# Kernel optimization log

Hardware: AMD Instinct MI355X
Metric: run time of the kernel (lower is better)

Reference implementation:

```python
import math
import jax
import jax.numpy as jnp
import numpy as np

N_IMG = 8
A = 3
H = 100
W = 100
STRIDE = 16
IMG = 1600
PRE_NMS_TOP_N = 2000
POST_NMS_TOP_N = 1000
NMS_THRESH = 0.7
MIN_SIZE = 0
BBOX_XFORM_CLIP = math.log(1000.0 / 16.0)


def setup_inputs() -> dict:
    key = jax.random.key(0)
    k1, k2 = jax.random.split(key)
    objectness = jax.random.normal(k1, (N_IMG, A, H, W), jnp.float32)
    box_regression = jax.random.normal(k2, (N_IMG, A * 4, H, W), jnp.float32) * 0.5
    # Grid anchors, flattened in (H, W, A) order to match objectness.permute(0,2,3,1)
    cy = (jnp.arange(H, dtype=jnp.float32) + 0.5) * STRIDE  # [H]
    cx = (jnp.arange(W, dtype=jnp.float32) + 0.5) * STRIDE  # [W]
    half = jnp.array([64.0, 128.0, 256.0], jnp.float32) / 2.0  # [A]
    cy = cy[:, None, None]  # [H,1,1]
    cx = cx[None, :, None]  # [1,W,1]
    s = half[None, None, :]  # [1,1,A]
    x1, y1, x2, y2 = jnp.broadcast_arrays(cx - s, cy - s, cx + s, cy + s)
    anc = jnp.stack([x1, y1, x2, y2], axis=-1).reshape(-1, 4)  # [H*W*A, 4]
    anchors = jnp.broadcast_to(anc[None], (N_IMG, H * W * A, 4)).copy()
    return {
        "objectness": objectness,
        "box_regression": box_regression,
        "anchors": anchors,
        "image_height": IMG,
        "image_width": IMG,
    }


def _decode(deltas, boxes):
    # BoxCoder(weights=(1,1,1,1)).decode with TO_REMOVE=1
    widths = boxes[..., 2] - boxes[..., 0] + 1.0
    heights = boxes[..., 3] - boxes[..., 1] + 1.0
    ctr_x = boxes[..., 0] + 0.5 * widths
    ctr_y = boxes[..., 1] + 0.5 * heights
    dx, dy = deltas[..., 0], deltas[..., 1]
    dw = jnp.minimum(deltas[..., 2], BBOX_XFORM_CLIP)
    dh = jnp.minimum(deltas[..., 3], BBOX_XFORM_CLIP)
    pcx = dx * widths + ctr_x
    pcy = dy * heights + ctr_y
    pw = jnp.exp(dw) * widths
    ph = jnp.exp(dh) * heights
    return jnp.stack(
        [pcx - 0.5 * pw, pcy - 0.5 * ph, pcx + 0.5 * pw - 1.0, pcy + 0.5 * ph - 1.0],
        axis=-1,
    )


def _nms_keep(boxes, valid, thresh):
    # boxes [n,4] sorted by descending score; valid: pre-filter mask.
    n = boxes.shape[0]
    x1, y1, x2, y2 = boxes[:, 0], boxes[:, 1], boxes[:, 2], boxes[:, 3]
    areas = (x2 - x1 + 1.0) * (y2 - y1 + 1.0)
    xx1 = jnp.maximum(x1[:, None], x1[None, :])
    yy1 = jnp.maximum(y1[:, None], y1[None, :])
    xx2 = jnp.minimum(x2[:, None], x2[None, :])
    yy2 = jnp.minimum(y2[:, None], y2[None, :])
    inter = jnp.maximum(xx2 - xx1 + 1.0, 0.0) * jnp.maximum(yy2 - yy1 + 1.0, 0.0)
    iou = inter / (areas[:, None] + areas[None, :] - inter)
    idx = jnp.arange(n)

    def body(i, keep):
        sup = keep[i] & (iou[i] > thresh) & (idx > i)
        return keep & ~sup

    return jax.lax.fori_loop(0, n, body, valid)


def _forward(objectness, box_regression, anchors, image_height, image_width):
    N, A_, H_, W_ = objectness.shape
    scores = jax.nn.sigmoid(objectness.transpose(0, 2, 3, 1).reshape(N, -1))  # [N, A*H*W]
    deltas = (
        box_regression.reshape(N, A_, 4, H_, W_)
        .transpose(0, 3, 4, 1, 2)
        .reshape(N, -1, 4)
    )
    pre = min(PRE_NMS_TOP_N, scores.shape[1])
    top_scores, top_idx = jax.lax.top_k(scores, pre)  # sorted descending
    deltas = jnp.take_along_axis(deltas, top_idx[:, :, None], axis=1)
    anc = jnp.take_along_axis(anchors, top_idx[:, :, None], axis=1)
    props = _decode(deltas, anc)  # [N, pre, 4]
    # clip to image (fact = 1)
    xs = jnp.clip(props[..., 0::2], 0.0, image_width - 1.0)
    ys = jnp.clip(props[..., 1::2], 0.0, image_height - 1.0)
    props = jnp.stack([xs[..., 0], ys[..., 0], xs[..., 1], ys[..., 1]], axis=-1)
    # filter small / out-of-image-center boxes
    ws = props[..., 2] - props[..., 0] + 1.0
    hs = props[..., 3] - props[..., 1] + 1.0
    xc = props[..., 0] + ws / 2.0
    yc = props[..., 1] + hs / 2.0
    valid = (ws >= MIN_SIZE) & (hs >= MIN_SIZE) & (xc < image_width) & (yc < image_height)
    keep = jax.vmap(lambda b, v: _nms_keep(b, v, NMS_THRESH))(props, valid)

    def _select(b, s, k):
        # compact kept boxes (already score-sorted) into fixed-size output
        rank = jnp.cumsum(k) - 1
        tgt = jnp.where(k & (rank < POST_NMS_TOP_N), rank, POST_NMS_TOP_N)
        ob = jnp.zeros((POST_NMS_TOP_N + 1, 4), b.dtype).at[tgt].set(b)[:POST_NMS_TOP_N]
        os = jnp.zeros((POST_NMS_TOP_N + 1,), s.dtype).at[tgt].set(s)[:POST_NMS_TOP_N]
        ov = jnp.arange(POST_NMS_TOP_N) < jnp.minimum(jnp.sum(k), POST_NMS_TOP_N)
        return ob, os, ov

    return jax.vmap(_select)(props, top_scores, keep)


def reference(objectness, box_regression, anchors, image_height, image_width):
    # Returns (boxes [N,post,4], objectness scores [N,post], valid mask [N,post])
    return _forward(objectness, box_regression, anchors, image_height, image_width)
```

## Files before the change

### kernel.cpp

```cpp
#include <hip/hip_runtime.h>
#include <math.h>
#include <stdint.h>

#define NIMG   8
#define NA     30000
#define NQ4    7500
#define PRE_N  2000
#define POST_N 1000
#define NMS_TH 0.7f
#define DCLIP  4.135166556742356f
#define IMGF   1600.0f
#define IMGM1  1599.0f
#define CAND_MAX 4096
#define HPITCH 4104
#define BIG_BIN 64
#define PREF_BIN 3064u


__device__ __forceinline__ void decode_store(
    uint64_t key, unsigned int rank, int n, const float* __restrict__ breg,
    float* __restrict__ wsBoxes, float* __restrict__ wsScores,
    int* __restrict__ wsValid)
{
    unsigned int idx = (unsigned int)key;
    unsigned int k   = ~((unsigned int)(key >> 32));
    unsigned int u   = (k & 0x80000000u) ? (k & 0x7fffffffu) : ~k;
    float logit = __uint_as_float(u);
    float score = 1.0f / (1.0f + expf(-logit));

    int a = idx % 3, t = idx / 3, w = t % 100, h = t / 100;
    const float* bp = breg + n*120000 + (a*4)*10000 + t;
    float dx = bp[0], dy = bp[10000], dw = bp[20000], dh = bp[30000];

    float half = (a == 0) ? 32.0f : ((a == 1) ? 64.0f : 128.0f);
    float cx = w * 16.0f + 8.0f, cy = h * 16.0f + 8.0f;
    float x1 = cx - half, y1 = cy - half, x2 = cx + half, y2 = cy + half;
    float wd = x2 - x1 + 1.0f, hg = y2 - y1 + 1.0f;
    float cxr = x1 + 0.5f * wd, cyr = y1 + 0.5f * hg;
    dw = fminf(dw, DCLIP); dh = fminf(dh, DCLIP);
    float pcx = dx * wd + cxr, pcy = dy * hg + cyr;
    float pw = expf(dw) * wd, ph = expf(dh) * hg;
    float px1 = pcx - 0.5f * pw, py1 = pcy - 0.5f * ph;
    float px2 = pcx + 0.5f * pw - 1.0f, py2 = pcy + 0.5f * ph - 1.0f;
    px1 = fminf(fmaxf(px1, 0.0f), IMGM1);
    px2 = fminf(fmaxf(px2, 0.0f), IMGM1);
    py1 = fminf(fmaxf(py1, 0.0f), IMGM1);
    py2 = fminf(fmaxf(py2, 0.0f), IMGM1);
    float wss = px2 - px1 + 1.0f, hss = py2 - py1 + 1.0f;
    float xc = px1 + wss * 0.5f, yc = py1 + hss * 0.5f;
    int valid = (wss >= 0.0f) && (hss >= 0.0f) && (xc < IMGF) && (yc < IMGF);

    ((float4*)wsBoxes)[n * PRE_N + (int)rank] = make_float4(px1, py1, px2, py2);
    wsScores[n * PRE_N + (int)rank] = score;
    wsValid [n * PRE_N + (int)rank] = valid;
}

__device__ __forceinline__ unsigned int keyof(float f) {
    unsigned int u = __float_as_uint(f);
    return (u & 0x80000000u) ? ~u : (u | 0x80000000u);
}

__global__ __launch_bounds__(1024) void topk_decode(
    const float* __restrict__ obj, const float* __restrict__ breg,
    float* __restrict__ wsBoxes, float* __restrict__ wsScores,
    int* __restrict__ wsValid)
{
    const int n    = blockIdx.x;
    const int tid  = threadIdx.x;
    const int lane = tid & 63;
    const int wid  = tid >> 6;
    const int rep  = wid & 3;

    __shared__ unsigned int   histf[4 * HPITCH];
    __shared__ unsigned short sufx[4096];
    __shared__ uint64_t       grp[CAND_MAX];
    __shared__ uint64_t       grp2[CAND_MAX];
    __shared__ unsigned int   wsum[16];
    __shared__ unsigned int   sbstar;
    __shared__ unsigned int   lbbase[16];
    __shared__ unsigned int   lbcnt, lbtot;

    unsigned int*   hist2  = histf;
    unsigned short* sufx2  = (unsigned short*)(histf + HPITCH);
    unsigned char*  bin2lb = (unsigned char*)(histf + 2 * HPITCH);

    for (int b = tid; b < 4 * HPITCH; b += 1024) histf[b] = 0u;
    __syncthreads();

    const float4* obj4 = (const float4*)(obj + n * NA);
    float4 v[8];
    #pragma unroll
    for (int kk = 0; kk < 7; ++kk) v[kk] = obj4[tid + kk * 1024];
    v[7] = make_float4(0.f, 0.f, 0.f, 0.f);
    if (tid < NQ4 - 7 * 1024) v[7] = obj4[tid + 7 * 1024];

    #pragma unroll
    for (int kk = 0; kk < 8; ++kk) {
        if (kk == 7 && tid >= NQ4 - 7 * 1024) continue;
        const float fv[4] = {v[kk].x, v[kk].y, v[kk].z, v[kk].w};
        #pragma unroll
        for (int e = 0; e < 4; ++e) {
            unsigned int b = keyof(fv[e]) >> 20;
            if (b >= PREF_BIN)
                atomicAdd(&histf[rep * HPITCH + b], 1u);
        }
    }
    __syncthreads();

    unsigned int c0, c1, c2, c3;
    {
        const int b0 = tid * 4;
        c0 = histf[b0+0] + histf[HPITCH+b0+0] + histf[2*HPITCH+b0+0] + histf[3*HPITCH+b0+0];
        c1 = histf[b0+1] + histf[HPITCH+b0+1] + histf[2*HPITCH+b0+1] + histf[3*HPITCH+b0+1];
        c2 = histf[b0+2] + histf[HPITCH+b0+2] + histf[2*HPITCH+b0+2] + histf[3*HPITCH+b0+2];
        c3 = histf[b0+3] + histf[HPITCH+b0+3] + histf[2*HPITCH+b0+3] + histf[3*HPITCH+b0+3];
    }
    unsigned int p = c0 + c1 + c2 + c3;
    unsigned int s = p;
    #pragma unroll
    for (int off = 1; off < 64; off <<= 1) {
        unsigned int vv = __shfl_down(s, off);
        if (lane + off < 64) s += vv;
    }
    if (lane == 0) wsum[wid] = s;
    __syncthreads();
    unsigned int ftotal = 0;
    for (int w = 0; w < 16; ++w) ftotal += wsum[w];

    if (ftotal < PRE_N) {
        #pragma unroll
        for (int kk = 0; kk < 8; ++kk) {
            if (kk == 7 && tid >= NQ4 - 7 * 1024) continue;
            const float fv[4] = {v[kk].x, v[kk].y, v[kk].z, v[kk].w};
            #pragma unroll
            for (int e = 0; e < 4; ++e) {
                unsigned int b = keyof(fv[e]) >> 20;
                if (b < PREF_BIN)
                    atomicAdd(&histf[rep * HPITCH + b], 1u);
            }
        }
        __syncthreads();
        {
            const int b0 = tid * 4;
            c0 = histf[b0+0] + histf[HPITCH+b0+0] + histf[2*HPITCH+b0+0] + histf[3*HPITCH+b0+0];
            c1 = histf[b0+1] + histf[HPITCH+b0+1] + histf[2*HPITCH+b0+1] + histf[3*HPITCH+b0+1];
            c2 = histf[b0+2] + histf[HPITCH+b0+2] + histf[2*HPITCH+b0+2] + histf[3*HPITCH+b0+2];
            c3 = histf[b0+3] + histf[HPITCH+b0+3] + histf[2*HPITCH+b0+3] + histf[3*HPITCH+b0+3];
        }
        p = c0 + c1 + c2 + c3;
        s = p;
        #pragma unroll
        for (int off = 1; off < 64; off <<= 1) {
            unsigned int vv = __shfl_down(s, off);
            if (lane + off < 64) s += vv;
        }
        __syncthreads();
        if (lane == 0) wsum[wid] = s;
        __syncthreads();
    }

    unsigned int wafter = 0;
    for (int w = wid + 1; w < 16; ++w) wafter += wsum[w];
    unsigned int after = (s - p) + wafter;
    {
        unsigned int S3 = after + c3;
        unsigned int S2 = S3 + c2;
        unsigned int S1 = S2 + c1;
        unsigned int S0 = S1 + c0;
        if (S3 >= PRE_N && after < PRE_N) { sbstar = tid*4+3; }
        if (S2 >= PRE_N && S3    < PRE_N) { sbstar = tid*4+2; }
        if (S1 >= PRE_N && S2    < PRE_N) { sbstar = tid*4+1; }
        if (S0 >= PRE_N && S1    < PRE_N) { sbstar = tid*4+0; }
        sufx[tid*4+0] = (unsigned short)S1;
        sufx[tid*4+1] = (unsigned short)S2;
        sufx[tid*4+2] = (unsigned short)S3;
        sufx[tid*4+3] = (unsigned short)after;

        const unsigned int st[4] = {S1, S2, S3, after};
        #pragma unroll
        for (int q = 0; q < 4; ++q) {
            const int b = tid*4 + q;
            unsigned int base = st[q];
            #pragma unroll
            for (int r = 0; r < 4; ++r) {
                unsigned int c = histf[r * HPITCH + b];
                histf[r * HPITCH + b] = base;
                base += c;
            }
        }
    }
    __syncthreads();
    const unsigned int bstar = sbstar;

    #pragma unroll
    for (int kk = 0; kk < 8; ++kk) {
        if (kk == 7 && tid >= NQ4 - 7 * 1024) continue;
        const float fv[4] = {v[kk].x, v[kk].y, v[kk].z, v[kk].w};
        #pragma unroll
        for (int e = 0; e < 4; ++e) {
            unsigned int k = keyof(fv[e]);
            unsigned int b = k >> 20;
            if (b < bstar) continue;
            int j = (tid + kk * 1024) * 4 + e;
            int a = j / 10000, t = j - a * 10000;
            uint64_t key = (((uint64_t)(~k)) << 32) | (unsigned int)(t * 3 + a);
            unsigned int slot = atomicAdd(&histf[rep * HPITCH + b], 1u);
            if (slot < CAND_MAX) grp[slot] = key;
        }
    }
    __syncthreads();

    const unsigned int total = min(histf[3 * HPITCH + bstar], (unsigned int)CAND_MAX);

    ((unsigned int*)bin2lb)[tid] = 0xFFFFFFFFu;
    hist2[tid] = 0u; hist2[tid+1024] = 0u; hist2[tid+2048] = 0u; hist2[tid+3072] = 0u;
    if (tid == 0) { lbcnt = 0u; lbtot = 0u; }
    __syncthreads();

    #pragma unroll
    for (int q = 0; q < 4; ++q) {
        const unsigned int b = (unsigned int)(tid*4 + q);
        if (b >= bstar) {
            const unsigned int ge  = min(histf[3*HPITCH + b], (unsigned int)CAND_MAX);
            const unsigned int cnt = ge - (unsigned int)sufx[b];
            if (cnt > (unsigned int)BIG_BIN) {
                unsigned int pos = atomicAdd(&lbcnt, 1u);
                if (pos < 16u) {
                    bin2lb[b] = (unsigned char)pos;
                    lbbase[pos] = atomicAdd(&lbtot, cnt);
                }
            }
        }
    }
    __syncthreads();

    for (unsigned int slot = tid; slot < total; slot += 1024) {
        const unsigned int hi = (unsigned int)(grp[slot] >> 32);
        const unsigned int b  = 4095u - (hi >> 20);
        const unsigned char lb = bin2lb[b];
        if (lb != 0xFFu)
            atomicAdd(&hist2[(unsigned int)lb * 256u + ((hi >> 12) & 0xFFu)], 1u);
    }
    __syncthreads();

    {
        const unsigned int nlb = min(lbcnt, 16u);
        if ((unsigned int)wid < nlb) {
            const int xb = wid * 256 + lane * 4;
            unsigned int e0 = hist2[xb+0], e1 = hist2[xb+1],
                         e2 = hist2[xb+2], e3 = hist2[xb+3];
            unsigned int tsum = e0 + e1 + e2 + e3;
            unsigned int inc = tsum;
            #pragma unroll
            for (int off = 1; off < 64; off <<= 1) {
                unsigned int vv = __shfl_up(inc, off);
                if (lane >= off) inc += vv;
            }
            unsigned int base = lbbase[wid] + (inc - tsum);
            hist2[xb+0] = base;             sufx2[xb+0] = (unsigned short)base;
            base += e0; hist2[xb+1] = base; sufx2[xb+1] = (unsigned short)base;
            base += e1; hist2[xb+2] = base; sufx2[xb+2] = (unsigned short)base;
            base += e2; hist2[xb+3] = base; sufx2[xb+3] = (unsigned short)base;
        }
    }
    __syncthreads();

    for (unsigned int slot = tid; slot < total; slot += 1024) {
        const uint64_t key = grp[slot];
        const unsigned int hi = (unsigned int)(key >> 32);
        const unsigned int b  = 4095u - (hi >> 20);
        const unsigned char lb = bin2lb[b];
        if (lb != 0xFFu) {
            unsigned int d = atomicAdd(&hist2[(unsigned int)lb * 256u + ((hi >> 12) & 0xFFu)], 1u);
            grp2[d] = key;
        }
    }
    __syncthreads();

    for (unsigned int slot = tid; slot < total; slot += 1024) {
        const uint64_t key = grp[slot];
        const unsigned int hi = (unsigned int)(key >> 32);
        const unsigned int b  = 4095u - (hi >> 20);
        const unsigned int gbeg = sufx[b];
        const unsigned int gend = min(histf[3 * HPITCH + b], (unsigned int)CAND_MAX);
        const unsigned char lb  = bin2lb[b];
        unsigned int rank;

        if (lb != 0xFFu) {
            const unsigned int x   = (unsigned int)lb * 256u + ((hi >> 12) & 0xFFu);
            const unsigned int s2  = sufx2[x];
            const unsigned int e2v = hist2[x];
            rank = gbeg + (s2 - lbbase[lb]);
            for (unsigned int g = s2; g < e2v; g += 8u) {
                #pragma unroll
                for (int i = 0; i < 8; ++i) {
                    const unsigned int gi = g + (unsigned int)i;
                    const uint64_t vv = grp2[min(gi, e2v - 1u)];
                    rank += (gi < e2v && vv < key) ? 1u : 0u;
                }
            }
        } else {
            rank = gbeg;
            unsigned int g = gbeg;
            for (; g + 8u <= gend; g += 8u) {
                uint64_t v0 = grp[g+0], v1 = grp[g+1], v2 = grp[g+2], v3 = grp[g+3];
                uint64_t v4 = grp[g+4], v5 = grp[g+5], v6 = grp[g+6], v7 = grp[g+7];
                unsigned int r0 = (v0 < key) ? 1u : 0u;
                r0 += (v1 < key) ? 1u : 0u;
                r0 += (v2 < key) ? 1u : 0u;
                r0 += (v3 < key) ? 1u : 0u;
                r0 += (v4 < key) ? 1u : 0u;
                r0 += (v5 < key) ? 1u : 0u;
                r0 += (v6 < key) ? 1u : 0u;
                r0 += (v7 < key) ? 1u : 0u;
                rank += r0;
            }
            for (; g < gend; ++g)
                rank += (grp[g] < key) ? 1u : 0u;
        }
        if (rank >= PRE_N) continue;
        decode_store(key, rank, n, breg, wsBoxes, wsScores, wsValid);
    }
}

__global__ __launch_bounds__(512) void nms_mask(
    const float* __restrict__ wsBoxes, uint64_t* __restrict__ mask)
{
    const int blk  = blockIdx.x;
    const int n    = blk >> 5;
    const int i_t  = blk & 31;
    const int tid  = threadIdx.x;
    const int lane = tid & 63;
    const int wv   = tid >> 6;

    __shared__ uint64_t tile[64 * 33];

    for (int idx = tid; idx < 64 * 33; idx += 512) tile[idx] = 0ull;
    __syncthreads();

    const int r = i_t * 64 + lane;
    float4 rb = (r < PRE_N) ? ((const float4*)wsBoxes)[n * PRE_N + r]
                            : make_float4(0.f, 0.f, 0.f, 0.f);
    float ra = (rb.z - rb.x + 1.0f) * (rb.w - rb.y + 1.0f);

    for (int j_t = i_t + wv; j_t < 32; j_t += 8) {
        const int j = j_t * 64 + lane;
        float4 cb = (j < PRE_N) ? ((const float4*)wsBoxes)[n * PRE_N + j]
                                : make_float4(3e30f, 3e30f, 3e30f, 3e30f);
        float ca = (cb.z - cb.x + 1.0f) * (cb.w - cb.y + 1.0f);
        const uint64_t jmask = (j_t == 31) ? 0xFFFFull : ~0ull;
        const bool diag = (j_t == i_t);
        uint64_t myword = 0ull;

        #pragma unroll
        for (int c = 0; c < 64; ++c) {
            float rx1 = __int_as_float(__builtin_amdgcn_readlane(__float_as_int(rb.x), c));
            float ry1 = __int_as_float(__builtin_amdgcn_readlane(__float_as_int(rb.y), c));
            float rx2 = __int_as_float(__builtin_amdgcn_readlane(__float_as_int(rb.z), c));
            float ry2 = __int_as_float(__builtin_amdgcn_readlane(__float_as_int(rb.w), c));
            float rar = __int_as_float(__builtin_amdgcn_readlane(__float_as_int(ra), c));
            float xx1 = fmaxf(rx1, cb.x), yy1 = fmaxf(ry1, cb.y);
            float xx2 = fminf(rx2, cb.z), yy2 = fminf(ry2, cb.w);
            float ww = fmaxf(xx2 - xx1 + 1.0f, 0.0f);
            float hh = fmaxf(yy2 - yy1 + 1.0f, 0.0f);
            float inter = ww * hh;
            float denom = rar + ca - inter;
            unsigned long long bits = __ballot(inter > NMS_TH * denom) & jmask;
            if (diag) bits &= (c == 63) ? 0ull : ((~0ull) << (c + 1));
            if (lane == c) myword = bits;
        }
        tile[lane * 33 + j_t] = myword;
    }
    __syncthreads();

    uint64_t* mrow = mask + ((size_t)n * PRE_N + (size_t)i_t * 64) * 32;
    const int cmax = (i_t == 31) ? 16 : 64;
    for (int idx = tid; idx < cmax * 32; idx += 512) {
        const int rr = idx >> 5, w = idx & 31;
        mrow[idx] = tile[rr * 33 + w];
    }
}

__global__ __launch_bounds__(512) void nms_scan_select(
    const float* __restrict__ wsBoxes, const float* __restrict__ wsScores,
    const int* __restrict__ wsValid, const uint64_t* __restrict__ mask,
    float* __restrict__ out)
{
    const int n    = blockIdx.x;
    const int tid  = threadIdx.x;
    const int lane = tid & 63;
    const int wid  = tid >> 6;

    __shared__ unsigned int sup[64];
    __shared__ unsigned int kml, kmh;
    __shared__ int skept, sdone;
    __shared__ int sscan[256];

    if (tid < 64) sup[tid] = 0u;
    if (tid == 0) { skept = 0; sdone = 0; }
    __syncthreads();

    if (tid < 500) {
        int4 vv = ((const int4*)(wsValid + n * PRE_N))[tid];
        unsigned int nib = (vv.x ? 0u : 1u) | ((vv.y ? 0u : 1u) << 1)
                         | ((vv.z ? 0u : 1u) << 2) | ((vv.w ? 0u : 1u) << 3);
        if (nib) atomicOr(&sup[tid >> 3], nib << ((tid & 7) * 4));
    } else {
        atomicOr(&sup[tid >> 3], 0xFu << ((tid & 7) * 4));
    }
    __syncthreads();

    const uint64_t* mrow = mask + (size_t)n * PRE_N * 32;

    unsigned int cl = 0u, ch = 0u;
    if (wid == 0) {
        uint64_t cw = (lane < PRE_N) ? mrow[(size_t)lane * 32 + 0] : 0ull;
        cl = (unsigned int)cw; ch = (unsigned int)(cw >> 32);
    }

    for (int g = 0; g < 32; ++g) {
        __syncthreads();
        if (sdone) break;

        if (wid == 0) {
            unsigned int nl = 0u, nh = 0u;
            if (g < 31) {
                const int r = (g + 1) * 64 + lane;
                uint64_t cw = (r < PRE_N) ? mrow[(size_t)r * 32 + (g + 1)] : 0ull;
                nl = (unsigned int)cw; nh = (unsigned int)(cw >> 32);
            }

            unsigned long long win =
                ((unsigned long long)sup[2*g + 1] << 32) | sup[2*g];
            #pragma unroll
            for (int b = 0; b < 64; ++b) {
                unsigned long long t =
                    ((unsigned long long)(unsigned int)__builtin_amdgcn_readlane((int)ch, b) << 32)
                    | (unsigned int)__builtin_amdgcn_readlane((int)cl, b);
                unsigned long long dead = (win >> b) & 1ull;
                win |= t & (dead - 1ull);
            }
            unsigned long long km = ~win;
            if (lane == 0) {
                sup[2*g]     = (unsigned int)win;
                sup[2*g + 1] = (unsigned int)(win >> 32);
                kml = (unsigned int)km;
                kmh = (unsigned int)(km >> 32);
                int nk = skept + __popcll(km);
                skept = nk;
                if (nk >= POST_N) sdone = 1;
            }
            cl = nl; ch = nh;
        }
        __syncthreads();

        if (!sdone) {
            const int w = tid & 31;
            if (w > g) {
                const unsigned long long km =
                    ((unsigned long long)kmh << 32) | kml;
                const int r0 = (tid >> 5) * 4;
                unsigned long long acc = 0ull;
                #pragma unroll
                for (int q = 0; q < 4; ++q) {
                    const int rl = r0 + q;
                    if ((km >> rl) & 1ull)
                        acc |= mrow[(size_t)(g * 64 + rl) * 32 + w];
                }
                if (acc) {
                    atomicOr(&sup[2*w],     (unsigned int)acc);
                    atomicOr(&sup[2*w + 1], (unsigned int)(acc >> 32));
                }
            }
        }
    }
    __syncthreads();

    int c[8];
    int lsum = 0;
    const int base8 = tid * 8;
    if (tid < 256) {
        for (int q = 0; q < 8; ++q) {
            const int i = base8 + q;
            c[q] = (i < PRE_N) ? (int)((~sup[i >> 5] >> (i & 31)) & 1u) : 0;
            lsum += c[q];
        }
        sscan[tid] = lsum;
    }
    __syncthreads();
    for (int off = 1; off < 256; off <<= 1) {
        int v = 0;
        if (tid < 256 && tid >= off) v = sscan[tid - off];
        __syncthreads();
        if (tid < 256) sscan[tid] += v;
        __syncthreads();
    }
    const int excl  = (tid < 256) ? (sscan[tid] - lsum) : 0;
    const int total = sscan[255];

    float* ob  = out + n * POST_N * 4;
    float* osc = out + NIMG * POST_N * 4 + n * POST_N;
    float* ovd = out + NIMG * POST_N * 5 + n * POST_N;

    for (int i = tid; i < POST_N * 4; i += 512) ob[i] = 0.0f;
    for (int i = tid; i < POST_N; i += 512) osc[i] = 0.0f;
    const int lim = min(total, POST_N);
    for (int i = tid; i < POST_N; i += 512) ovd[i] = (i < lim) ? 1.0f : 0.0f;
    __syncthreads();

    if (tid < 256) {
        int run = excl;
        for (int q = 0; q < 8; ++q) {
            const int i = base8 + q;
            if (i < PRE_N && c[q]) {
                if (run < POST_N) {
                    float4 b = ((const float4*)wsBoxes)[n * PRE_N + i];
                    ob[run * 4 + 0] = b.x;
                    ob[run * 4 + 1] = b.y;
                    ob[run * 4 + 2] = b.z;
                    ob[run * 4 + 3] = b.w;
                    osc[run] = wsScores[n * PRE_N + i];
                }
                run++;
            }
        }
    }
}

extern "C" void kernel_launch(void* const* d_in, const int* in_sizes, int n_in,
                              void* d_out, int out_size, void* d_ws, size_t ws_size,
                              hipStream_t stream) {
    const float* obj  = (const float*)d_in[0];
    const float* breg = (const float*)d_in[1];
    float* ws        = (float*)d_ws;
    float* wsBoxes   = ws;
    float* wsScores  = ws + 64000;
    int*   wsValid   = (int*)(ws + 80000);
    uint64_t* wsMask = (uint64_t*)(ws + 96000);

    topk_decode<<<NIMG, 1024, 0, stream>>>(obj, breg, wsBoxes, wsScores, wsValid);
    nms_mask<<<NIMG * 32, 512, 0, stream>>>(wsBoxes, wsMask);
    nms_scan_select<<<NIMG, 512, 0, stream>>>(wsBoxes, wsScores, wsValid, wsMask,
                                              (float*)d_out);
}
```

Baseline: 169.5 us.

## Prefetch NMS mask rows one group ahead and hand-code serial scan in scalar asm

Each thread now loads its four mask words for the next 64-row group one iteration early, so the global loads overlap the serial suppression scan instead of stalling after the barrier. The 64-step serial scan over the diagonal block is written as inline scalar assembly (readlane, bitcmp, cselect, and/or) to keep the running window in SGPRs and avoid 64-bit vector emulation. The prefetch loads every mask word unconditionally rather than only the kept rows, and the inline asm adds maintenance and correctness risk.

```diff
diff --git a/kernel.cpp b/kernel.cpp
--- a/kernel.cpp
+++ b/kernel.cpp
@@ -381,6 +381,26 @@
     }
 }
 
+#define NSA(b) \
+    "v_readlane_b32 %[tlo], %[cl], " #b "\n\t" \
+    "v_readlane_b32 %[thi], %[ch], " #b "\n\t" \
+    "s_bitcmp1_b32 %[wlo], " #b "\n\t" \
+    "s_cselect_b32 %[m], 0, -1\n\t" \
+    "s_and_b32 %[tlo], %[tlo], %[m]\n\t" \
+    "s_and_b32 %[thi], %[thi], %[m]\n\t" \
+    "s_or_b32 %[wlo], %[wlo], %[tlo]\n\t" \
+    "s_or_b32 %[whi], %[whi], %[thi]\n\t"
+
+#define NSB(b, c) \
+    "v_readlane_b32 %[tlo], %[cl], " #b "\n\t" \
+    "v_readlane_b32 %[thi], %[ch], " #b "\n\t" \
+    "s_bitcmp1_b32 %[whi], " #c "\n\t" \
+    "s_cselect_b32 %[m], 0, -1\n\t" \
+    "s_and_b32 %[tlo], %[tlo], %[m]\n\t" \
+    "s_and_b32 %[thi], %[thi], %[m]\n\t" \
+    "s_or_b32 %[wlo], %[wlo], %[tlo]\n\t" \
+    "s_or_b32 %[whi], %[whi], %[thi]\n\t"
+
 __global__ __launch_bounds__(512) void nms_scan_select(
     const float* __restrict__ wsBoxes, const float* __restrict__ wsScores,
     const int* __restrict__ wsValid, const uint64_t* __restrict__ mask,
@@ -412,6 +432,15 @@
 
     const uint64_t* mrow = mask + (size_t)n * PRE_N * 32;
 
+    const int r0 = (tid >> 5) * 4;
+    const int w  = tid & 31;
+    uint64_t pfc[4], pfn[4];
+    #pragma unroll
+    for (int q = 0; q < 4; ++q) {
+        const int r = r0 + q;
+        pfn[q] = (w > 0 && r < PRE_N) ? mrow[(size_t)r * 32 + w] : 0ull;
+    }
+
     unsigned int cl = 0u, ch = 0u;
     if (wid == 0) {
         uint64_t cw = (lane < PRE_N) ? mrow[(size_t)lane * 32 + 0] : 0ull;
@@ -421,6 +450,16 @@
     for (int g = 0; g < 32; ++g) {
         __syncthreads();
         if (sdone) break;
+
+        #pragma unroll
+        for (int q = 0; q < 4; ++q) pfc[q] = pfn[q];
+        if (g < 31) {
+            #pragma unroll
+            for (int q = 0; q < 4; ++q) {
+                const int r = (g + 1) * 64 + r0 + q;
+                pfn[q] = (w > g + 1 && r < PRE_N) ? mrow[(size_t)r * 32 + w] : 0ull;
+            }
+        }
 
         if (wid == 0) {
             unsigned int nl = 0u, nh = 0u;
@@ -430,23 +469,33 @@
                 nl = (unsigned int)cw; nh = (unsigned int)(cw >> 32);
             }
 
-            unsigned long long win =
-                ((unsigned long long)sup[2*g + 1] << 32) | sup[2*g];
-            #pragma unroll
-            for (int b = 0; b < 64; ++b) {
-                unsigned long long t =
-                    ((unsigned long long)(unsigned int)__builtin_amdgcn_readlane((int)ch, b) << 32)
-                    | (unsigned int)__builtin_amdgcn_readlane((int)cl, b);
-                unsigned long long dead = (win >> b) & 1ull;
-                win |= t & (dead - 1ull);
-            }
-            unsigned long long km = ~win;
+            unsigned int wlo = (unsigned int)__builtin_amdgcn_readfirstlane((int)sup[2*g]);
+            unsigned int whi = (unsigned int)__builtin_amdgcn_readfirstlane((int)sup[2*g+1]);
+            int tlo_, thi_, m_;
+            asm volatile(
+                NSA(0)  NSA(1)  NSA(2)  NSA(3)  NSA(4)  NSA(5)  NSA(6)  NSA(7)
+                NSA(8)  NSA(9)  NSA(10) NSA(11) NSA(12) NSA(13) NSA(14) NSA(15)
+                NSA(16) NSA(17) NSA(18) NSA(19) NSA(20) NSA(21) NSA(22) NSA(23)
+                NSA(24) NSA(25) NSA(26) NSA(27) NSA(28) NSA(29) NSA(30) NSA(31)
+                NSB(32,0)  NSB(33,1)  NSB(34,2)  NSB(35,3)
+                NSB(36,4)  NSB(37,5)  NSB(38,6)  NSB(39,7)
+                NSB(40,8)  NSB(41,9)  NSB(42,10) NSB(43,11)
+                NSB(44,12) NSB(45,13) NSB(46,14) NSB(47,15)
+                NSB(48,16) NSB(49,17) NSB(50,18) NSB(51,19)
+                NSB(52,20) NSB(53,21) NSB(54,22) NSB(55,23)
+                NSB(56,24) NSB(57,25) NSB(58,26) NSB(59,27)
+                NSB(60,28) NSB(61,29) NSB(62,30) NSB(63,31)
+                : [wlo]"+s"(wlo), [whi]"+s"(whi),
+                  [tlo]"=&s"(tlo_), [thi]"=&s"(thi_), [m]"=&s"(m_)
+                : [cl]"v"(cl), [ch]"v"(ch)
+                : "scc");
+
             if (lane == 0) {
-                sup[2*g]     = (unsigned int)win;
-                sup[2*g + 1] = (unsigned int)(win >> 32);
-                kml = (unsigned int)km;
-                kmh = (unsigned int)(km >> 32);
-                int nk = skept + __popcll(km);
+                sup[2*g]     = wlo;
+                sup[2*g + 1] = whi;
+                unsigned int kl = ~wlo, kh = ~whi;
+                kml = kl; kmh = kh;
+                int nk = skept + __popc(kl) + __popc(kh);
                 skept = nk;
                 if (nk >= POST_N) sdone = 1;
             }
@@ -454,23 +503,17 @@
         }
         __syncthreads();
 
-        if (!sdone) {
-            const int w = tid & 31;
-            if (w > g) {
-                const unsigned long long km =
-                    ((unsigned long long)kmh << 32) | kml;
-                const int r0 = (tid >> 5) * 4;
-                unsigned long long acc = 0ull;
-                #pragma unroll
-                for (int q = 0; q < 4; ++q) {
-                    const int rl = r0 + q;
-                    if ((km >> rl) & 1ull)
-                        acc |= mrow[(size_t)(g * 64 + rl) * 32 + w];
-                }
-                if (acc) {
-                    atomicOr(&sup[2*w],     (unsigned int)acc);
-                    atomicOr(&sup[2*w + 1], (unsigned int)(acc >> 32));
-                }
+        if (!sdone && w > g) {
+            const unsigned long long km =
+                ((unsigned long long)kmh << 32) | kml;
+            unsigned long long acc = 0ull;
+            #pragma unroll
+            for (int q = 0; q < 4; ++q) {
+                if ((km >> (r0 + q)) & 1ull) acc |= pfc[q];
+            }
+            if (acc) {
+                atomicOr(&sup[2*w],     (unsigned int)acc);
+                atomicOr(&sup[2*w + 1], (unsigned int)(acc >> 32));
             }
         }
     }
```

After: 151.5 us (median of 2 runs). 1.12x faster.
